# Performance work log

Hardware: AMD Instinct MI355X
Metric: run time of the kernel (lower is better)

The kernel has to match this reference:

```python
import jax, jax.numpy as jnp
import numpy as np

D = 256; NH = 8; NL = 4; NP = 4; DFF = 1024; BS = 8; NQ = 300
DH = D // NH
EPS = 1e-5
SPATIAL = np.array([[100, 150], [50, 75], [25, 38], [13, 19]], dtype=np.int64)  # (H, W) per level
SIZES = (SPATIAL[:, 0] * SPATIAL[:, 1])
S = int(SIZES.sum())  # 19947
LSI = np.concatenate([[0], np.cumsum(SIZES)[:-1]]).astype(np.int64)


def setup_inputs() -> dict:
    key = jax.random.key(0)
    ks = iter(jax.random.split(key, 48))
    def nrm(shape, s=0.02):
        return jax.random.normal(next(ks), shape, jnp.float32) * s
    return {
        "tgt": jax.random.normal(next(ks), (BS, NQ, D), jnp.float32),
        "tgt_query_pos": jax.random.normal(next(ks), (BS, NQ, D), jnp.float32),
        "tgt_reference_points": jax.random.uniform(next(ks), (BS, NQ, NL, 2), jnp.float32),
        "memory": jax.random.normal(next(ks), (BS, S, D), jnp.float32),
        "memory_key_padding_mask": jnp.zeros((BS, S), jnp.bool_),
        "memory_spatial_shapes": jnp.asarray(SPATIAL),
        "memory_level_start_index": jnp.asarray(LSI),
        # self-attention (nn.MultiheadAttention) params
        "in_proj_w": nrm((3 * D, D)), "in_proj_b": jnp.zeros((3 * D,), jnp.float32),
        "out_proj_w": nrm((D, D)), "out_proj_b": jnp.zeros((D,), jnp.float32),
        # layernorms
        "norm1_g": jnp.ones((D,), jnp.float32), "norm1_b": jnp.zeros((D,), jnp.float32),
        "norm2_g": jnp.ones((D,), jnp.float32), "norm2_b": jnp.zeros((D,), jnp.float32),
        "norm3_g": jnp.ones((D,), jnp.float32), "norm3_b": jnp.zeros((D,), jnp.float32),
        # MSDeformAttn params
        "samp_off_w": nrm((NH * NL * NP * 2, D)), "samp_off_b": nrm((NH * NL * NP * 2,), 0.5),
        "attn_wt_w": nrm((NH * NL * NP, D)), "attn_wt_b": jnp.zeros((NH * NL * NP,), jnp.float32),
        "value_w": nrm((D, D)), "value_b": jnp.zeros((D,), jnp.float32),
        "outp_w": nrm((D, D)), "outp_b": jnp.zeros((D,), jnp.float32),
        # FFN params
        "lin1_w": nrm((DFF, D)), "lin1_b": jnp.zeros((DFF,), jnp.float32),
        "lin2_w": nrm((D, DFF)), "lin2_b": jnp.zeros((D,), jnp.float32),
    }


def _ln(x, g, b):
    m = x.mean(-1, keepdims=True)
    v = ((x - m) ** 2).mean(-1, keepdims=True)
    return (x - m) / jnp.sqrt(v + EPS) * g + b


def _self_attn(tgt, pos, in_w, in_b, ow, ob):
    bs, nq, _ = tgt.shape
    qk = tgt + pos
    qw, kw, vw = jnp.split(in_w, 3, axis=0)
    qb, kb, vb = jnp.split(in_b, 3)
    proj = lambda x, w, b: (x @ w.T + b).reshape(bs, nq, NH, DH)
    qh, kh, vh = proj(qk, qw, qb), proj(qk, kw, kb), proj(tgt, vw, vb)
    logits = jnp.einsum('bqhd,bkhd->bhqk', qh, kh) / np.sqrt(DH).astype(np.float32)
    a = jax.nn.softmax(logits, axis=-1)
    o = jnp.einsum('bhqk,bkhd->bqhd', a, vh).reshape(bs, nq, D)
    return o @ ow.T + ob


def _msdeform(query, ref, memory, pad_mask, so_w, so_b, aw_w, aw_b, vw, vb, ow, ob):
    bs, nq, _ = query.shape
    value = memory @ vw.T + vb
    value = jnp.where(pad_mask[..., None], 0.0, value).reshape(bs, S, NH, DH)
    off = (query @ so_w.T + so_b).reshape(bs, nq, NH, NL, NP, 2)
    aw = jax.nn.softmax((query @ aw_w.T + aw_b).reshape(bs, nq, NH, NL * NP), axis=-1)
    aw = aw.reshape(bs, nq, NH, NL, NP)
    # offset normalizer is (W, H) per level
    normalizer = jnp.asarray(SPATIAL[:, ::-1].copy(), jnp.float32)
    locs = ref[:, :, None, :, None, :] + off / normalizer[None, None, None, :, None, :]
    out = jnp.zeros((bs, nq, NH, DH), jnp.float32)
    for l in range(NL):
        Hl, Wl = int(SPATIAL[l, 0]), int(SPATIAL[l, 1])
        s0 = int(LSI[l])
        v = value[:, s0:s0 + Hl * Wl]  # [bs, Hl*Wl, NH, DH]
        # grid_sample(align_corners=False) pixel mapping
        x = locs[:, :, :, l, :, 0] * Wl - 0.5  # [bs, nq, NH, NP]
        y = locs[:, :, :, l, :, 1] * Hl - 0.5
        x0f, y0f = jnp.floor(x), jnp.floor(y)
        tx, ty = x - x0f, y - y0f
        x0, y0 = x0f.astype(jnp.int32), y0f.astype(jnp.int32)
        samp = jnp.zeros(x.shape + (DH,), jnp.float32)
        for dy, dx, w in ((0, 0, (1 - ty) * (1 - tx)), (0, 1, (1 - ty) * tx),
                          (1, 0, ty * (1 - tx)), (1, 1, ty * tx)):
            xi, yi = x0 + dx, y0 + dy
            valid = (xi >= 0) & (xi < Wl) & (yi >= 0) & (yi < Hl)  # zero padding
            idx = jnp.clip(yi, 0, Hl - 1) * Wl + jnp.clip(xi, 0, Wl - 1)
            idx2 = idx.swapaxes(2, 3).reshape(bs, nq * NP, NH)
            g = jnp.take_along_axis(v, idx2[..., None], axis=1)  # [bs, nq*NP, NH, DH]
            g = g.reshape(bs, nq, NP, NH, DH).transpose(0, 1, 3, 2, 4)
            samp = samp + g * (w * valid)[..., None]
        out = out + jnp.einsum('bqhp,bqhpd->bqhd', aw[:, :, :, l], samp)
    return out.reshape(bs, nq, D) @ ow.T + ob


def reference(tgt, tgt_query_pos, tgt_reference_points, memory, memory_key_padding_mask,
              memory_spatial_shapes, memory_level_start_index,
              in_proj_w, in_proj_b, out_proj_w, out_proj_b,
              norm1_g, norm1_b, norm2_g, norm2_b, norm3_g, norm3_b,
              samp_off_w, samp_off_b, attn_wt_w, attn_wt_b,
              value_w, value_b, outp_w, outp_b,
              lin1_w, lin1_b, lin2_w, lin2_b):
    # self-cross ordering (self_cross=True), eval mode (dropout=identity)
    t2 = _self_attn(tgt, tgt_query_pos, in_proj_w, in_proj_b, out_proj_w, out_proj_b)
    tgt = _ln(tgt + t2, norm2_g, norm2_b)
    t2 = _msdeform(tgt + tgt_query_pos, tgt_reference_points, memory, memory_key_padding_mask,
                   samp_off_w, samp_off_b, attn_wt_w, attn_wt_b, value_w, value_b, outp_w, outp_b)
    tgt = _ln(tgt + t2, norm1_g, norm1_b)
    t2 = jax.nn.relu(tgt @ lin1_w.T + lin1_b) @ lin2_w.T + lin2_b
    return _ln(tgt + t2, norm3_g, norm3_b)
```

## Files before the change

### kernel.cpp

```cpp
#include <hip/hip_runtime.h>
#include <hip/hip_bf16.h>

#define D_   256
#define NH_  8
#define NL_  4
#define NP_  4
#define DFF_ 1024
#define BS_  8
#define NQ_  300
#define DH_  32
#define S_TOT 19947
#define EPS_ 1e-5f

typedef __bf16 bf16x8 __attribute__((ext_vector_type(8)));
typedef __bf16 bf16x4 __attribute__((ext_vector_type(4)));
typedef float  f32x4  __attribute__((ext_vector_type(4)));

#define W_INW  0
#define W_OUTW 196608
#define W_SOW  262144
#define W_AWW  327680
#define W_VW   360448
#define W_OPW  425984
#define W_L1W  491520
#define W_L2W  753664
#define W_TOT  1015808

__global__ __launch_bounds__(256) void cast_w_kernel(
    const float* __restrict__ s_inw, const float* __restrict__ s_outw,
    const float* __restrict__ s_sow, const float* __restrict__ s_aww,
    const float* __restrict__ s_vw,  const float* __restrict__ s_opw,
    const float* __restrict__ s_l1w, const float* __restrict__ s_l2w,
    __bf16* __restrict__ dst, __bf16* __restrict__ Wf)
{
    if (blockIdx.x >= 992) {
        const int g = (blockIdx.x - 992) * 256 + threadIdx.x;
        const int l = g & 63;
        const int t = (g >> 6) & 15;
        const int s = g >> 10;
        const int row = t * 16 + (l & 15);
        const int col = s * 32 + (l >> 4) * 8;
        const float* src = s_vw + (size_t)row * 256 + col;
        const float4 v0 = *(const float4*)src;
        const float4 v1 = *(const float4*)(src + 4);
        bf16x8 o;
        o[0] = (__bf16)v0.x; o[1] = (__bf16)v0.y;
        o[2] = (__bf16)v0.z; o[3] = (__bf16)v0.w;
        o[4] = (__bf16)v1.x; o[5] = (__bf16)v1.y;
        o[6] = (__bf16)v1.z; o[7] = (__bf16)v1.w;
        *(bf16x8*)(Wf + (size_t)g * 8) = o;
        return;
    }
    const int i = (blockIdx.x * 256 + threadIdx.x) * 4;
    if (i >= W_TOT) return;
    const float* s; int off;
    if      (i < W_OUTW) { s = s_inw;  off = W_INW;  }
    else if (i < W_SOW)  { s = s_outw; off = W_OUTW; }
    else if (i < W_AWW)  { s = s_sow;  off = W_SOW;  }
    else if (i < W_VW)   { s = s_aww;  off = W_AWW;  }
    else if (i < W_OPW)  { s = s_vw;   off = W_VW;   }
    else if (i < W_L1W)  { s = s_opw;  off = W_OPW;  }
    else if (i < W_L2W)  { s = s_l1w;  off = W_L1W;  }
    else                 { s = s_l2w;  off = W_L2W;  }
    const float4 v = *(const float4*)(s + (i - off));
    bf16x4 o;
    o[0] = (__bf16)v.x; o[1] = (__bf16)v.y;
    o[2] = (__bf16)v.z; o[3] = (__bf16)v.w;
    *(bf16x4*)(dst + i) = o;
}

__global__ __launch_bounds__(512, 4) void gemm_value(
    const float* __restrict__ A, const __bf16* __restrict__ Wf,
    const float* __restrict__ bias, __hip_bfloat16* __restrict__ C, int M)
{
    __shared__ __align__(16) __bf16 As[2][16][264];
    const int tid = threadIdx.x;
    const int wave = tid >> 6, lane = tid & 63;
    const int frow = lane & 15;
    const int k8 = (lane >> 4) * 8;

    bf16x8 bB[2][8];
#pragma unroll
    for (int j = 0; j < 2; ++j) {
        const int t = wave * 2 + j;
#pragma unroll
        for (int s = 0; s < 8; ++s)
            bB[j][s] = *(const bf16x8*)(Wf + ((size_t)(s * 16 + t) * 64 + lane) * 8);
    }
    float bb0 = bias[wave * 32 + frow];
    float bb1 = bias[wave * 32 + 16 + frow];

    const int nt = (M + 15) >> 4;
    const int stride = gridDim.x;
    int tile = blockIdx.x;

    const int srow = tid >> 5;
    const int scol = (tid & 31) * 8;

    {
        int gr = tile * 16 + srow; if (gr >= M) gr = M - 1;
        const float* ap = A + (size_t)gr * 256 + scol;
        const float4 a0 = *(const float4*)ap;
        const float4 a1 = *(const float4*)(ap + 4);
        bf16x8 o;
        o[0] = (__bf16)a0.x; o[1] = (__bf16)a0.y;
        o[2] = (__bf16)a0.z; o[3] = (__bf16)a0.w;
        o[4] = (__bf16)a1.x; o[5] = (__bf16)a1.y;
        o[6] = (__bf16)a1.z; o[7] = (__bf16)a1.w;
        *(bf16x8*)&As[0][srow][scol] = o;
    }
    __syncthreads();

    int buf = 0;
    for (; tile < nt; tile += stride, buf ^= 1) {
        const int nxt = tile + stride;
        const bool have_nxt = nxt < nt;
        float4 p0, p1;
        if (have_nxt) {
            int gr = nxt * 16 + srow; if (gr >= M) gr = M - 1;
            const float* ap = A + (size_t)gr * 256 + scol;
            p0 = *(const float4*)ap;
            p1 = *(const float4*)(ap + 4);
        }

        f32x4 acc0 = (f32x4){0.f, 0.f, 0.f, 0.f};
        f32x4 acc1 = acc0;
#pragma unroll
        for (int s = 0; s < 8; ++s) {
            const bf16x8 aF = *(const bf16x8*)&As[buf][frow][s * 32 + k8];
            acc0 = __builtin_amdgcn_mfma_f32_16x16x32_bf16(aF, bB[0][s], acc0, 0, 0, 0);
            acc1 = __builtin_amdgcn_mfma_f32_16x16x32_bf16(aF, bB[1][s], acc1, 0, 0, 0);
        }

        const int m0 = tile * 16;
        const int row0 = (lane >> 4) * 4;
#pragma unroll
        for (int r = 0; r < 4; ++r) {
            const int gr = m0 + row0 + r;
            if (gr < M) {
                const int bb_ = gr / S_TOT;
                const int ss_ = gr - bb_ * S_TOT;
                __hip_bfloat16* cp =
                    C + (((size_t)bb_ * 8 + wave) * S_TOT + ss_) * 32 + frow;
                cp[0]  = __float2bfloat16(acc0[r] + bb0);
                cp[16] = __float2bfloat16(acc1[r] + bb1);
            }
        }

        if (have_nxt) {
            bf16x8 o;
            o[0] = (__bf16)p0.x; o[1] = (__bf16)p0.y;
            o[2] = (__bf16)p0.z; o[3] = (__bf16)p0.w;
            o[4] = (__bf16)p1.x; o[5] = (__bf16)p1.y;
            o[6] = (__bf16)p1.z; o[7] = (__bf16)p1.w;
            *(bf16x8*)&As[buf ^ 1][srow][scol] = o;
        }
        __syncthreads();
    }
}

__global__ __launch_bounds__(256) void gemm_small(
    const float* __restrict__ A, const float* __restrict__ A2,
    const __bf16* __restrict__ W, const float* __restrict__ bias,
    float* __restrict__ C, int M, int N, int K, int relu,
    const float* __restrict__ bias2, float* __restrict__ C2, int N1, int a2_all)
{
    __shared__ __align__(16) __bf16 As[64][40];
    __shared__ __align__(16) __bf16 Bs[64][40];
    const int tid = threadIdx.x;
    const int wave = tid >> 6, lane = tid & 63;
    const int m0 = blockIdx.x * 64, n0 = blockIdx.y * 64;
    const int frow = lane & 15, fk = (lane >> 4) * 8;

    f32x4 acc[4];
#pragma unroll
    for (int j = 0; j < 4; ++j) acc[j] = (f32x4){0.f, 0.f, 0.f, 0.f};

    const int ar = tid >> 2;
    const int ak = (tid & 3) * 8;
    const bool a_ok = (m0 + ar) < M;
    const bool use_a2 = (A2 != nullptr) && (a2_all || n0 < N1);

    for (int k0 = 0; k0 < K; k0 += 32) {
        float4 a0 = make_float4(0,0,0,0), a1 = a0;
        if (a_ok) {
            const float* ap = A + (size_t)(m0 + ar) * K + k0 + ak;
            a0 = *(const float4*)ap;
            a1 = *(const float4*)(ap + 4);
            if (use_a2) {
                const float* ap2 = A2 + (size_t)(m0 + ar) * K + k0 + ak;
                const float4 c0 = *(const float4*)ap2;
                const float4 c1 = *(const float4*)(ap2 + 4);
                a0.x += c0.x; a0.y += c0.y; a0.z += c0.z; a0.w += c0.w;
                a1.x += c1.x; a1.y += c1.y; a1.z += c1.z; a1.w += c1.w;
            }
        }
        const bf16x8 b8 = *(const bf16x8*)(W + (size_t)(n0 + ar) * K + k0 + ak);

        __syncthreads();
        bf16x8 w0;
        w0[0] = (__bf16)a0.x; w0[1] = (__bf16)a0.y; w0[2] = (__bf16)a0.z; w0[3] = (__bf16)a0.w;
        w0[4] = (__bf16)a1.x; w0[5] = (__bf16)a1.y; w0[6] = (__bf16)a1.z; w0[7] = (__bf16)a1.w;
        *(bf16x8*)&As[ar][ak] = w0;
        *(bf16x8*)&Bs[ar][ak] = b8;
        __syncthreads();

        const bf16x8 aF = *(const bf16x8*)&As[wave * 16 + frow][fk];
#pragma unroll
        for (int j = 0; j < 4; ++j) {
            const bf16x8 bF = *(const bf16x8*)&Bs[j * 16 + frow][fk];
            acc[j] = __builtin_amdgcn_mfma_f32_16x16x32_bf16(aF, bF, acc[j], 0, 0, 0);
        }
    }

    const int row = m0 + wave * 16 + (lane >> 4) * 4;
#pragma unroll
    for (int j = 0; j < 4; ++j) {
        const int col = n0 + j * 16 + frow;
        float* dst; const float* bsrc; int strideC, ccol;
        if (!C2 || col < N1) { dst = C;  bsrc = bias;  strideC = N1;     ccol = col; }
        else                 { dst = C2; bsrc = bias2; strideC = N - N1; ccol = col - N1; }
        const float bb = bsrc[ccol];
#pragma unroll
        for (int r = 0; r < 4; ++r) {
            if (row + r >= M) continue;
            float val = acc[j][r] + bb;
            if (relu) val = fmaxf(val, 0.f);
            dst[(size_t)(row + r) * strideC + ccol] = val;
        }
    }
}

__global__ __launch_bounds__(256) void attn_fused_kernel(
    const float* __restrict__ qk, const float* __restrict__ v,
    float* __restrict__ attn)
{
    __shared__ __align__(16) __bf16 Vt[32][328];
    __shared__ __align__(16) __bf16 Ps[64][328];
    const int qt = blockIdx.x, bh = blockIdx.y;
    const int b = bh >> 3, h = bh & 7;
    const int tid = threadIdx.x;
    const int wave = tid >> 6, lane = tid & 63;
    const float scale = 0.17677669529663687f;

    {
        const int d = tid & 31;
        for (int kk = tid >> 5; kk < NQ_; kk += 8)
            Vt[d][kk] = (__bf16)v[(size_t)(b * NQ_ + kk) * 256 + h * 32 + d];
        for (int i = tid; i < 32 * 20; i += 256)
            Vt[i & 31][300 + (i >> 5)] = (__bf16)0.f;
        for (int i = tid; i < 64 * 16; i += 256)
            Ps[i & 63][304 + (i >> 6)] = (__bf16)0.f;
    }

    const int m = qt * 64 + wave * 16 + (lane & 15);
    const int k8 = (lane >> 4) * 8;

    bf16x8 aF = {};
    if (m < NQ_) {
        const float* qp = qk + (size_t)(b * NQ_ + m) * 512 + h * 32 + k8;
        const float4 q0 = *(const float4*)qp;
        const float4 q1 = *(const float4*)(qp + 4);
        aF[0] = (__bf16)q0.x; aF[1] = (__bf16)q0.y;
        aF[2] = (__bf16)q0.z; aF[3] = (__bf16)q0.w;
        aF[4] = (__bf16)q1.x; aF[5] = (__bf16)q1.y;
        aF[6] = (__bf16)q1.z; aF[7] = (__bf16)q1.w;
    }

    f32x4 c[19];
#pragma unroll
    for (int t = 0; t < 19; ++t) {
        const int n = t * 16 + (lane & 15);
        bf16x8 bF = {};
        if (n < NQ_) {
            const float* kp = qk + (size_t)(b * NQ_ + n) * 512 + 256 + h * 32 + k8;
            const float4 k0 = *(const float4*)kp;
            const float4 k1 = *(const float4*)(kp + 4);
            bF[0] = (__bf16)k0.x; bF[1] = (__bf16)k0.y;
            bF[2] = (__bf16)k0.z; bF[3] = (__bf16)k0.w;
            bF[4] = (__bf16)k1.x; bF[5] = (__bf16)k1.y;
            bF[6] = (__bf16)k1.z; bF[7] = (__bf16)k1.w;
        }
        f32x4 z = (f32x4){0.f, 0.f, 0.f, 0.f};
        c[t] = __builtin_amdgcn_mfma_f32_16x16x32_bf16(aF, bF, z, 0, 0, 0);
    }

    const int myc = lane & 15;
#pragma unroll
    for (int t = 0; t < 19; ++t) {
        const bool ok = (t * 16 + myc) < NQ_;
#pragma unroll
        for (int r = 0; r < 4; ++r)
            c[t][r] = ok ? c[t][r] * scale : -1e30f;
    }

    float mx[4] = {-1e30f, -1e30f, -1e30f, -1e30f};
#pragma unroll
    for (int t = 0; t < 19; ++t)
#pragma unroll
        for (int r = 0; r < 4; ++r) mx[r] = fmaxf(mx[r], c[t][r]);
#pragma unroll
    for (int off = 8; off; off >>= 1)
#pragma unroll
        for (int r = 0; r < 4; ++r)
            mx[r] = fmaxf(mx[r], __shfl_xor(mx[r], off, 64));

    float sum[4] = {0.f, 0.f, 0.f, 0.f};
#pragma unroll
    for (int t = 0; t < 19; ++t)
#pragma unroll
        for (int r = 0; r < 4; ++r) {
            const float e = __expf(c[t][r] - mx[r]);
            c[t][r] = e;
            sum[r] += e;
        }
#pragma unroll
    for (int off = 8; off; off >>= 1)
#pragma unroll
        for (int r = 0; r < 4; ++r)
            sum[r] += __shfl_xor(sum[r], off, 64);
    float inv[4];
#pragma unroll
    for (int r = 0; r < 4; ++r) inv[r] = 1.f / sum[r];

    const int lrow0 = wave * 16 + (lane >> 4) * 4;
#pragma unroll
    for (int t = 0; t < 19; ++t) {
        const int col = t * 16 + myc;
#pragma unroll
        for (int r = 0; r < 4; ++r)
            Ps[lrow0 + r][col] = (__bf16)(c[t][r] * inv[r]);
    }
    __syncthreads();

    const int lm = wave * 16 + (lane & 15);
    f32x4 acc0 = (f32x4){0.f, 0.f, 0.f, 0.f};
    f32x4 acc1 = acc0;
#pragma unroll
    for (int k0 = 0; k0 < 320; k0 += 32) {
        const bf16x8 pF = *(const bf16x8*)&Ps[lm][k0 + k8];
        const bf16x8 b0 = *(const bf16x8*)&Vt[lane & 15][k0 + k8];
        const bf16x8 b1 = *(const bf16x8*)&Vt[16 + (lane & 15)][k0 + k8];
        acc0 = __builtin_amdgcn_mfma_f32_16x16x32_bf16(pF, b0, acc0, 0, 0, 0);
        acc1 = __builtin_amdgcn_mfma_f32_16x16x32_bf16(pF, b1, acc1, 0, 0, 0);
    }

    const int row0 = qt * 64 + lrow0;
    const int col = lane & 15;
#pragma unroll
    for (int r = 0; r < 4; ++r) {
        if (row0 + r >= NQ_) continue;
        float* op = attn + (size_t)(b * NQ_ + row0 + r) * 256 + h * 32;
        op[col]      = acc0[r];
        op[col + 16] = acc1[r];
    }
}

__global__ __launch_bounds__(256) void ln_kernel(
    const float* __restrict__ x, const float* __restrict__ res,
    const float* __restrict__ g, const float* __restrict__ bt,
    float* __restrict__ out,
    const float* __restrict__ pos, float* __restrict__ out2)
{
    const int row = blockIdx.x;
    const int tid = threadIdx.x;
    const size_t idx = (size_t)row * D_ + tid;
    float v = x[idx] + (res ? res[idx] : 0.f);

    __shared__ float red[4];
    float s = v;
#pragma unroll
    for (int off = 32; off; off >>= 1) s += __shfl_xor(s, off, 64);
    if ((tid & 63) == 0) red[tid >> 6] = s;
    __syncthreads();
    const float mean = (red[0] + red[1] + red[2] + red[3]) * (1.f / D_);
    const float c = v - mean;
    __syncthreads();

    float s2 = c * c;
#pragma unroll
    for (int off = 32; off; off >>= 1) s2 += __shfl_xor(s2, off, 64);
    if ((tid & 63) == 0) red[tid >> 6] = s2;
    __syncthreads();
    const float var = (red[0] + red[1] + red[2] + red[3]) * (1.f / D_);

    const float y = c * rsqrtf(var + EPS_) * g[tid] + bt[tid];
    out[idx] = y;
    if (out2) out2[idx] = y + pos[idx];
}

__global__ __launch_bounds__(256) void msdeform_kernel(
    const float* __restrict__ offs, const float* __restrict__ awl,
    const float* __restrict__ refp, const __hip_bfloat16* __restrict__ value,
    float* __restrict__ samp)
{
    const int rsec = threadIdx.x >> 6;
    const int row = blockIdx.x * 4 + rsec;
    const int b = row / NQ_;
    const int t = threadIdx.x & 63;
    const int h = t >> 3, d4 = t & 7;

    __shared__ float off_s[4][256];
    __shared__ float aw_s[4][128];
    __shared__ float ref_s[4][8];
    off_s[rsec][t]       = offs[(size_t)row * 256 + t];
    off_s[rsec][t + 64]  = offs[(size_t)row * 256 + t + 64];
    off_s[rsec][t + 128] = offs[(size_t)row * 256 + t + 128];
    off_s[rsec][t + 192] = offs[(size_t)row * 256 + t + 192];
    aw_s[rsec][t]        = awl[(size_t)row * 128 + t];
    aw_s[rsec][t + 64]   = awl[(size_t)row * 128 + t + 64];
    if (t < 8) ref_s[rsec][t] = refp[(size_t)row * 8 + t];
    __syncthreads();

    float mx = -1e30f;
#pragma unroll
    for (int i = 0; i < 16; ++i) mx = fmaxf(mx, aw_s[rsec][h * 16 + i]);
    float sum = 0.f;
#pragma unroll
    for (int i = 0; i < 16; ++i) sum += __expf(aw_s[rsec][h * 16 + i] - mx);
    const float winv = 1.f / sum;

    const int Hs[4] = {100, 50, 25, 13};
    const int Wl_[4] = {150, 75, 38, 19};
    const int S0[4] = {0, 15000, 18750, 19700};

    float o0 = 0.f, o1 = 0.f, o2 = 0.f, o3 = 0.f;
    const __hip_bfloat16* vbase =
        value + ((size_t)(b * 8 + h) * S_TOT) * 32 + d4 * 4;

#pragma unroll
    for (int l = 0; l < NL_; ++l) {
        const int Hl = Hs[l], Wl = Wl_[l];
        const float rx = ref_s[rsec][l * 2], ry = ref_s[rsec][l * 2 + 1];
        const __hip_bfloat16* vl = vbase + (size_t)S0[l] * 32;
#pragma unroll
        for (int p = 0; p < NP_; ++p) {
            const int oi = ((h * NL_ + l) * NP_ + p) * 2;
            const float lx = rx + off_s[rsec][oi] / (float)Wl;
            const float ly = ry + off_s[rsec][oi + 1] / (float)Hl;
            const float x = lx * Wl - 0.5f;
            const float y = ly * Hl - 0.5f;
            const float x0f = floorf(x), y0f = floorf(y);
            const float tx = x - x0f, ty = y - y0f;
            const int x0 = (int)x0f, y0 = (int)y0f;
            const float aw = __expf(aw_s[rsec][h * 16 + l * 4 + p] - mx) * winv;

            float s0 = 0.f, s1 = 0.f, s2 = 0.f, s3 = 0.f;
#pragma unroll
            for (int cc = 0; cc < 4; ++cc) {
                const int dy = cc >> 1, dx = cc & 1;
                const int xi = x0 + dx, yi = y0 + dy;
                const float w = (dy ? ty : 1.f - ty) * (dx ? tx : 1.f - tx);
                if (xi >= 0 && xi < Wl && yi >= 0 && yi < Hl) {
                    const int idx = yi * Wl + xi;
                    const uint2 u = *(const uint2*)(vl + (size_t)idx * 32);
                    s0 += w * __uint_as_float(u.x << 16);
                    s1 += w * __uint_as_float(u.x & 0xffff0000u);
                    s2 += w * __uint_as_float(u.y << 16);
                    s3 += w * __uint_as_float(u.y & 0xffff0000u);
                }
            }
            o0 += aw * s0;
            o1 += aw * s1;
            o2 += aw * s2;
            o3 += aw * s3;
        }
    }
    float4 ov; ov.x = o0; ov.y = o1; ov.z = o2; ov.w = o3;
    *(float4*)(samp + (size_t)row * 256 + h * 32 + d4 * 4) = ov;
}

extern "C" void kernel_launch(void* const* d_in, const int* in_sizes, int n_in,
                              void* d_out, int out_size, void* d_ws, size_t ws_size,
                              hipStream_t stream)
{
    const float* tgt   = (const float*)d_in[0];
    const float* pos   = (const float*)d_in[1];
    const float* refp  = (const float*)d_in[2];
    const float* memory= (const float*)d_in[3];
    const float* in_w  = (const float*)d_in[7];
    const float* in_b  = (const float*)d_in[8];
    const float* outw  = (const float*)d_in[9];
    const float* outb  = (const float*)d_in[10];
    const float* n1g = (const float*)d_in[11]; const float* n1b = (const float*)d_in[12];
    const float* n2g = (const float*)d_in[13]; const float* n2b = (const float*)d_in[14];
    const float* n3g = (const float*)d_in[15]; const float* n3b = (const float*)d_in[16];
    const float* sow = (const float*)d_in[17]; const float* sob = (const float*)d_in[18];
    const float* aww = (const float*)d_in[19]; const float* awb = (const float*)d_in[20];
    const float* vw  = (const float*)d_in[21]; const float* vb_ = (const float*)d_in[22];
    const float* opw = (const float*)d_in[23]; const float* opb = (const float*)d_in[24];
    const float* l1w = (const float*)d_in[25]; const float* l1b = (const float*)d_in[26];
    const float* l2w = (const float*)d_in[27]; const float* l2b = (const float*)d_in[28];
    float* out = (float*)d_out;

    char* ws = (char*)d_ws;
    size_t o = 0;
    auto alloc = [&](size_t bytes) -> char* {
        char* p = ws + o;
        o += (bytes + 255) & ~(size_t)255;
        return p;
    };

    const int M = BS_ * NQ_;
    __bf16* Wb = (__bf16*)alloc((size_t)W_TOT * 2);
    __bf16* Wf = (__bf16*)alloc((size_t)65536 * 2);
    __hip_bfloat16* value = (__hip_bfloat16*)alloc((size_t)BS_ * S_TOT * D_ * 2);
    float* qk    = (float*)alloc((size_t)M * 512 * 4);
    float* v     = (float*)alloc((size_t)M * 256 * 4);
    float* attn  = (float*)alloc((size_t)M * 256 * 4);
    float* attno = (float*)alloc((size_t)M * 256 * 4);
    float* tgt1  = (float*)alloc((size_t)M * 256 * 4);
    float* offs  = (float*)alloc((size_t)M * 256 * 4);
    float* awl   = (float*)alloc((size_t)M * 128 * 4);
    float* samp  = (float*)alloc((size_t)M * 256 * 4);
    float* t2m   = (float*)alloc((size_t)M * 256 * 4);
    float* tgt2  = (float*)alloc((size_t)M * 256 * 4);
    float* ffn1  = (float*)alloc((size_t)M * 1024 * 4);
    float* ffn2  = (float*)alloc((size_t)M * 256 * 4);

    const dim3 blk(256);
    const int MB = (M + 63) / 64;

    cast_w_kernel<<<1024, blk, 0, stream>>>(
        in_w, outw, sow, aww, vw, opw, l1w, l2w, Wb, Wf);

    gemm_small<<<dim3(MB, 12), blk, 0, stream>>>(
        tgt, pos, Wb + W_INW, in_b, qk, M, 768, 256, 0, in_b + 512, v, 512, 0);

    attn_fused_kernel<<<dim3(5, 64), blk, 0, stream>>>(qk, v, attn);

    gemm_small<<<dim3(MB, 4), blk, 0, stream>>>(
        attn, nullptr, Wb + W_OUTW, outb, attno, M, 256, 256, 0, nullptr, nullptr, 256, 0);

    ln_kernel<<<M, blk, 0, stream>>>(tgt, attno, n2g, n2b, tgt1, nullptr, nullptr);

    gemm_small<<<dim3(MB, 6), blk, 0, stream>>>(
        tgt1, pos, Wb + W_SOW, sob, offs, M, 384, 256, 0, awb, awl, 256, 1);

    gemm_value<<<dim3(512), dim3(512), 0, stream>>>(memory, Wf, vb_, value, BS_ * S_TOT);

    msdeform_kernel<<<M / 4, blk, 0, stream>>>(offs, awl, refp, value, samp);

    gemm_small<<<dim3(MB, 4), blk, 0, stream>>>(
        samp, nullptr, Wb + W_OPW, opb, t2m, M, 256, 256, 0, nullptr, nullptr, 256, 0);

    ln_kernel<<<M, blk, 0, stream>>>(tgt1, t2m, n1g, n1b, tgt2, nullptr, nullptr);

    gemm_small<<<dim3(MB, 16), blk, 0, stream>>>(
        tgt2, nullptr, Wb + W_L1W, l1b, ffn1, M, 1024, 256, 1, nullptr, nullptr, 1024, 0);

    gemm_small<<<dim3(MB, 4), blk, 0, stream>>>(
        ffn1, nullptr, Wb + W_L2W, l2b, ffn2, M, 256, 1024, 0, nullptr, nullptr, 256, 0);

    ln_kernel<<<M, blk, 0, stream>>>(tgt2, ffn2, n3g, n3b, out, nullptr, nullptr);
}
```

Baseline: 436.3 us.

## Merge self-attn in-projection GEMM and memory value projection into one launch

Combines the QKV in-projection GEMM and the large memory value-projection GEMM into a single kernel, using block-index ranges to pick which work a block does. The in-projection blocks run two 64-column tiles per 512-thread block, and the value blocks keep the existing persistent loop. This removes one launch and lets the small in-projection work overlap with the bandwidth-bound value GEMM instead of running serially. The cost is heavier launch bounds for the in-proj path, half the threads idle during A staging, and shared-memory aliasing between the two roles.

```diff
diff --git a/kernel.cpp b/kernel.cpp
--- a/kernel.cpp
+++ b/kernel.cpp
@@ -25,6 +25,9 @@
 #define W_L1W  491520
 #define W_L2W  753664
 #define W_TOT  1015808
+
+#define NB_INPROJ 228
+#define NB_GV     512
 
 __global__ __launch_bounds__(256) void cast_w_kernel(
     const float* __restrict__ s_inw, const float* __restrict__ s_outw,
@@ -69,12 +72,93 @@
     *(bf16x4*)(dst + i) = o;
 }
 
-__global__ __launch_bounds__(512, 4) void gemm_value(
-    const float* __restrict__ A, const __bf16* __restrict__ Wf,
-    const float* __restrict__ bias, __hip_bfloat16* __restrict__ C, int M)
+__global__ __launch_bounds__(512, 4) void inproj_value_kernel(
+    const float* __restrict__ A, const float* __restrict__ A2,
+    const __bf16* __restrict__ W, const float* __restrict__ bias,
+    float* __restrict__ C, const float* __restrict__ bias2,
+    float* __restrict__ C2, int M,
+    const float* __restrict__ Av, const __bf16* __restrict__ Wf,
+    const float* __restrict__ biasv, __hip_bfloat16* __restrict__ Cv, int Mv)
 {
-    __shared__ __align__(16) __bf16 As[2][16][264];
+    __shared__ __align__(16) char smem[17408];
     const int tid = threadIdx.x;
+
+    if (blockIdx.x < NB_INPROJ) {
+        __bf16 (*As)[40] = (__bf16(*)[40])smem;
+        __bf16 (*Bs)[64][40] = (__bf16(*)[64][40])(smem + 5120);
+
+        const int half = tid >> 8;
+        const int t = tid & 255;
+        const int m0 = (blockIdx.x / 6) * 64;
+        const int pair = blockIdx.x % 6;
+        const int n0 = (pair * 2 + half) * 64;
+        const int wv = (tid >> 6) & 3;
+        const int lane = tid & 63;
+        const int frow = lane & 15, fk = (lane >> 4) * 8;
+        const int K = 256, N = 768, N1 = 512;
+
+        f32x4 acc[4];
+#pragma unroll
+        for (int j = 0; j < 4; ++j) acc[j] = (f32x4){0.f, 0.f, 0.f, 0.f};
+
+        const int ar = t >> 2;
+        const int ak = (t & 3) * 8;
+        const bool a_ok = (half == 0) && (m0 + ar) < M;
+        const bool use_a2 = (n0 < N1);
+
+        for (int k0 = 0; k0 < K; k0 += 32) {
+            float4 a0 = make_float4(0,0,0,0), a1 = a0;
+            if (a_ok) {
+                const float* ap = A + (size_t)(m0 + ar) * K + k0 + ak;
+                a0 = *(const float4*)ap;
+                a1 = *(const float4*)(ap + 4);
+                if (use_a2 || (pair * 128 < N1)) {}
+            }
+            if (a_ok && (pair < 4)) {
+                const float* ap2 = A2 + (size_t)(m0 + ar) * K + k0 + ak;
+                const float4 c0 = *(const float4*)ap2;
+                const float4 c1 = *(const float4*)(ap2 + 4);
+                a0.x += c0.x; a0.y += c0.y; a0.z += c0.z; a0.w += c0.w;
+                a1.x += c1.x; a1.y += c1.y; a1.z += c1.z; a1.w += c1.w;
+            }
+            const bf16x8 b8 = *(const bf16x8*)(W + (size_t)(n0 + ar) * K + k0 + ak);
+
+            __syncthreads();
+            if (half == 0) {
+                bf16x8 w0;
+                w0[0] = (__bf16)a0.x; w0[1] = (__bf16)a0.y; w0[2] = (__bf16)a0.z; w0[3] = (__bf16)a0.w;
+                w0[4] = (__bf16)a1.x; w0[5] = (__bf16)a1.y; w0[6] = (__bf16)a1.z; w0[7] = (__bf16)a1.w;
+                *(bf16x8*)&As[ar][ak] = w0;
+            }
+            *(bf16x8*)&Bs[half][ar][ak] = b8;
+            __syncthreads();
+
+            const bf16x8 aF = *(const bf16x8*)&As[wv * 16 + frow][fk];
+#pragma unroll
+            for (int j = 0; j < 4; ++j) {
+                const bf16x8 bF = *(const bf16x8*)&Bs[half][j * 16 + frow][fk];
+                acc[j] = __builtin_amdgcn_mfma_f32_16x16x32_bf16(aF, bF, acc[j], 0, 0, 0);
+            }
+        }
+
+        const int row = m0 + wv * 16 + (lane >> 4) * 4;
+#pragma unroll
+        for (int j = 0; j < 4; ++j) {
+            const int col = n0 + j * 16 + frow;
+            float* dst; const float* bsrc; int strideC, ccol;
+            if (col < N1) { dst = C;  bsrc = bias;  strideC = N1;     ccol = col; }
+            else          { dst = C2; bsrc = bias2; strideC = N - N1; ccol = col - N1; }
+            const float bb = bsrc[ccol];
+#pragma unroll
+            for (int r = 0; r < 4; ++r) {
+                if (row + r >= M) continue;
+                dst[(size_t)(row + r) * strideC + ccol] = acc[j][r] + bb;
+            }
+        }
+        return;
+    }
+
+    __bf16 (*Asv)[16][264] = (__bf16(*)[16][264])smem;
     const int wave = tid >> 6, lane = tid & 63;
     const int frow = lane & 15;
     const int k8 = (lane >> 4) * 8;
@@ -87,19 +171,19 @@
         for (int s = 0; s < 8; ++s)
             bB[j][s] = *(const bf16x8*)(Wf + ((size_t)(s * 16 + t) * 64 + lane) * 8);
     }
-    float bb0 = bias[wave * 32 + frow];
-    float bb1 = bias[wave * 32 + 16 + frow];
-
-    const int nt = (M + 15) >> 4;
-    const int stride = gridDim.x;
-    int tile = blockIdx.x;
+    float bb0 = biasv[wave * 32 + frow];
+    float bb1 = biasv[wave * 32 + 16 + frow];
+
+    const int nt = (Mv + 15) >> 4;
+    const int stride = NB_GV;
+    int tile = blockIdx.x - NB_INPROJ;
 
     const int srow = tid >> 5;
     const int scol = (tid & 31) * 8;
 
     {
-        int gr = tile * 16 + srow; if (gr >= M) gr = M - 1;
-        const float* ap = A + (size_t)gr * 256 + scol;
+        int gr = tile * 16 + srow; if (gr >= Mv) gr = Mv - 1;
+        const float* ap = Av + (size_t)gr * 256 + scol;
         const float4 a0 = *(const float4*)ap;
         const float4 a1 = *(const float4*)(ap + 4);
         bf16x8 o;
@@ -107,7 +191,7 @@
         o[2] = (__bf16)a0.z; o[3] = (__bf16)a0.w;
         o[4] = (__bf16)a1.x; o[5] = (__bf16)a1.y;
         o[6] = (__bf16)a1.z; o[7] = (__bf16)a1.w;
-        *(bf16x8*)&As[0][srow][scol] = o;
+        *(bf16x8*)&Asv[0][srow][scol] = o;
     }
     __syncthreads();
 
@@ -117,8 +201,8 @@
         const bool have_nxt = nxt < nt;
         float4 p0, p1;
         if (have_nxt) {
-            int gr = nxt * 16 + srow; if (gr >= M) gr = M - 1;
-            const float* ap = A + (size_t)gr * 256 + scol;
+            int gr = nxt * 16 + srow; if (gr >= Mv) gr = Mv - 1;
+            const float* ap = Av + (size_t)gr * 256 + scol;
             p0 = *(const float4*)ap;
             p1 = *(const float4*)(ap + 4);
         }
@@ -127,7 +211,7 @@
         f32x4 acc1 = acc0;
 #pragma unroll
         for (int s = 0; s < 8; ++s) {
-            const bf16x8 aF = *(const bf16x8*)&As[buf][frow][s * 32 + k8];
+            const bf16x8 aF = *(const bf16x8*)&Asv[buf][frow][s * 32 + k8];
             acc0 = __builtin_amdgcn_mfma_f32_16x16x32_bf16(aF, bB[0][s], acc0, 0, 0, 0);
             acc1 = __builtin_amdgcn_mfma_f32_16x16x32_bf16(aF, bB[1][s], acc1, 0, 0, 0);
         }
@@ -137,11 +221,11 @@
 #pragma unroll
         for (int r = 0; r < 4; ++r) {
             const int gr = m0 + row0 + r;
-            if (gr < M) {
+            if (gr < Mv) {
                 const int bb_ = gr / S_TOT;
                 const int ss_ = gr - bb_ * S_TOT;
                 __hip_bfloat16* cp =
-                    C + (((size_t)bb_ * 8 + wave) * S_TOT + ss_) * 32 + frow;
+                    Cv + (((size_t)bb_ * 8 + wave) * S_TOT + ss_) * 32 + frow;
                 cp[0]  = __float2bfloat16(acc0[r] + bb0);
                 cp[16] = __float2bfloat16(acc1[r] + bb1);
             }
@@ -153,7 +237,7 @@
             o[2] = (__bf16)p0.z; o[3] = (__bf16)p0.w;
             o[4] = (__bf16)p1.x; o[5] = (__bf16)p1.y;
             o[6] = (__bf16)p1.z; o[7] = (__bf16)p1.w;
-            *(bf16x8*)&As[buf ^ 1][srow][scol] = o;
+            *(bf16x8*)&Asv[buf ^ 1][srow][scol] = o;
         }
         __syncthreads();
     }
@@ -524,8 +608,9 @@
     cast_w_kernel<<<1024, blk, 0, stream>>>(
         in_w, outw, sow, aww, vw, opw, l1w, l2w, Wb, Wf);
 
-    gemm_small<<<dim3(MB, 12), blk, 0, stream>>>(
-        tgt, pos, Wb + W_INW, in_b, qk, M, 768, 256, 0, in_b + 512, v, 512, 0);
+    inproj_value_kernel<<<dim3(NB_INPROJ + NB_GV), dim3(512), 0, stream>>>(
+        tgt, pos, Wb + W_INW, in_b, qk, in_b + 512, v, M,
+        memory, Wf, vb_, value, BS_ * S_TOT);
 
     attn_fused_kernel<<<dim3(5, 64), blk, 0, stream>>>(qk, v, attn);
 
@@ -537,8 +622,6 @@
     gemm_small<<<dim3(MB, 6), blk, 0, stream>>>(
         tgt1, pos, Wb + W_SOW, sob, offs, M, 384, 256, 0, awb, awl, 256, 1);
 
-    gemm_value<<<dim3(512), dim3(512), 0, stream>>>(memory, Wf, vb_, value, BS_ * S_TOT);
-
     msdeform_kernel<<<M / 4, blk, 0, stream>>>(offs, awl, refp, value, samp);
 
     gemm_small<<<dim3(MB, 4), blk, 0, stream>>>(
```

After: 435.1 us. About the same (-0.3%).
